# Optimization experiments

Measured on AMD Instinct MI355X. Metric: run time of the kernel, lower is better.

Reference implementation:

```python
import jax, jax.numpy as jnp
import numpy as np

P_PARTS = 6
NUM_CLASSES = 50000
BATCH = 128
PART_DIM = 256
LABEL_SMOOTH = 0.1
MARGIN = 0.3
TEMP = 3.0
KL_CLAMP = 5.0
LAMBDA_GRAPH = 0.1
LAMBDA_TRI = 1.0
LAMBDA_ADV = 0.1
START_EPOCH = 20


def setup_inputs() -> dict:
    key = jax.random.key(0)
    ks = jax.random.split(key, 8)
    id_logits = jax.random.normal(ks[0], (P_PARTS, BATCH, NUM_CLASSES), dtype=jnp.float32)
    id_features = jax.random.normal(ks[1], (P_PARTS, BATCH, PART_DIM), dtype=jnp.float32)
    gray_features = jax.random.normal(ks[2], (P_PARTS, BATCH, PART_DIM), dtype=jnp.float32)
    # soft labels are probability distributions (teacher softmax outputs)
    soft_labels = jax.nn.softmax(jax.random.normal(ks[3], (P_PARTS, BATCH, NUM_CLASSES), dtype=jnp.float32), axis=-1)
    entropy_weights = jax.random.uniform(ks[4], (P_PARTS, BATCH), dtype=jnp.float32)
    adv_logits = jax.random.normal(ks[5], (P_PARTS, BATCH, 2), dtype=jnp.float32)
    labels = jax.random.randint(ks[6], (BATCH,), 0, 16, dtype=jnp.int64 if jax.config.jax_enable_x64 else jnp.int32)
    modality_labels = jax.random.randint(ks[7], (BATCH,), 0, 2, dtype=jnp.int64 if jax.config.jax_enable_x64 else jnp.int32)
    return {
        'id_logits': id_logits,
        'id_features': id_features,
        'gray_features': gray_features,
        'soft_labels': soft_labels,
        'entropy_weights': entropy_weights,
        'adv_logits': adv_logits,
        'labels': labels,
        'modality_labels': modality_labels,
        'current_epoch': 25,
    }


def _ce(logits, labels, smoothing):
    # torch CrossEntropyLoss with label_smoothing, mean reduction. logits: [B,C]
    logp = jax.nn.log_softmax(logits, axis=-1)
    nll = -jnp.take_along_axis(logp, labels[:, None], axis=-1)[:, 0]
    smooth = -jnp.mean(logp, axis=-1)
    return jnp.mean((1.0 - smoothing) * nll + smoothing * smooth)


def _triplet(feat, target_feat, labels, same):
    # euclidean cdist [B,B]
    sq = (jnp.sum(feat * feat, axis=1)[:, None]
          + jnp.sum(target_feat * target_feat, axis=1)[None, :]
          - 2.0 * feat @ target_feat.T)
    dist = jnp.sqrt(jnp.clip(sq, 0.0) + 1e-12)
    eq = labels[:, None] == labels[None, :]
    is_neg = ~eq
    is_pos = eq & (~jnp.eye(feat.shape[0], dtype=bool)) if same else eq
    # vectorized hard mining (replaces per-row python loop)
    dist_ap = jnp.where(is_pos.any(axis=1),
                        jnp.max(jnp.where(is_pos, dist, -jnp.inf), axis=1), 0.0)
    dist_an = jnp.where(is_neg.any(axis=1),
                        jnp.min(jnp.where(is_neg, dist, jnp.inf), axis=1), 1e6)
    # MarginRankingLoss with y=1: mean(relu(dist_ap - dist_an + margin))
    return jnp.mean(jnp.maximum(dist_ap - dist_an + MARGIN, 0.0))


def reference(id_logits, id_features, gray_features, soft_labels, entropy_weights,
              adv_logits, labels, modality_labels, current_epoch):
    P = id_logits.shape[0]
    # --- multi-part ID loss ---
    L_id = jnp.mean(jax.vmap(lambda lg: _ce(lg, labels, LABEL_SMOOTH))(id_logits))
    # --- triplet on L2-normalized concatenated part features ---
    feat = jnp.concatenate(list(id_features), axis=1)  # [B, P*D]
    feat = feat / jnp.linalg.norm(feat, axis=1, keepdims=True)
    L_tri = _triplet(feat, feat, labels, same=True)
    feat_gray = jnp.concatenate(list(gray_features), axis=1)
    feat_gray = feat_gray / jnp.linalg.norm(feat_gray, axis=1, keepdims=True)
    L_trans = _triplet(feat, feat_gray, labels, same=False)
    L_tri = L_tri + 0.5 * L_trans
    # --- graph distillation (KL) ---
    if current_epoch >= START_EPOCH:
        logp = jax.nn.log_softmax(id_logits / TEMP, axis=-1)  # [P,B,C]
        kl = jnp.sum(soft_labels * (jnp.log(soft_labels) - logp), axis=-1)  # [P,B]
        kl = jnp.minimum(kl, KL_CLAMP)
        L_graph = jnp.sum(jnp.mean(kl * entropy_weights, axis=1)) * (TEMP ** 2) / P
    else:
        L_graph = jnp.float32(0.0)
    # --- adversarial CE ---
    logp_adv = jax.nn.log_softmax(adv_logits, axis=-1)  # [P,B,2]
    nll_adv = -jnp.take_along_axis(logp_adv, modality_labels[None, :, None], axis=-1)[..., 0]
    L_adv = jnp.mean(jnp.mean(nll_adv, axis=1))
    total = L_id + LAMBDA_TRI * L_tri + LAMBDA_GRAPH * L_graph + LAMBDA_ADV * L_adv
    return total
```

## Files before the change

kernel.cpp:

```cpp
#include <hip/hip_runtime.h>

#define NCLS   50000
#define NC4    12500
#define BATCH  128
#define PPARTS 6
#define NROWS  768
#define FD     1536

__device__ __forceinline__ float wave_sum(float v) {
#pragma unroll
  for (int off = 32; off > 0; off >>= 1) v += __shfl_xor(v, off, 64);
  return v;
}

#define WS_INVF 16
#define WS_INVG 144
#define WS_D    272

__device__ __forceinline__ void chunk_update(float4 xv, float4 sv,
    float& m, float& e1, float& e2, float& sx, float& ss, float& ssl, float& ssx) {
  const float i3 = 1.0f / 3.0f;
  float cm = fmaxf(fmaxf(xv.x, xv.y), fmaxf(xv.z, xv.w));
  float nm = fmaxf(m, cm);
  float d0 = xv.x - nm, d1 = xv.y - nm, d2 = xv.z - nm, d3 = xv.w - nm;
  float r = m - nm;
  e1 = fmaf(e1, __expf(r),
            (__expf(d0) + __expf(d1)) + (__expf(d2) + __expf(d3)));
  e2 = fmaf(e2, __expf(r * i3),
            (__expf(d0 * i3) + __expf(d1 * i3)) + (__expf(d2 * i3) + __expf(d3 * i3)));
  m = nm;
  sx += (xv.x + xv.y) + (xv.z + xv.w);
  ss += (sv.x + sv.y) + (sv.z + sv.w);
  ssl = fmaf(sv.x, __logf(sv.x), fmaf(sv.y, __logf(sv.y),
        fmaf(sv.z, __logf(sv.z), fmaf(sv.w, __logf(sv.w), ssl))));
  ssx = fmaf(sv.x, xv.x, fmaf(sv.y, xv.y,
        fmaf(sv.z, xv.z, fmaf(sv.w, xv.w, ssx))));
}

__global__ __launch_bounds__(512) void big_rows_k(
    const float* __restrict__ X, const float* __restrict__ S,
    const float* __restrict__ W, const int* __restrict__ labels,
    float* __restrict__ acc) {
  const int row = blockIdx.x;
  const int b = row & (BATCH - 1);
  const int t = threadIdx.x;
  const size_t base = (size_t)row * NCLS;
  const float4* x4 = (const float4*)(X + base);
  const float4* s4 = (const float4*)(S + base);
  const float i3 = 1.0f / 3.0f;

  float x_lab = (t == 0) ? X[base + labels[b]] : 0.0f;

  float m = -1e30f, e1 = 0.0f, e2 = 0.0f;
  float sx = 0.0f, ss = 0.0f, ssl = 0.0f, ssx = 0.0f;

#pragma unroll 4
  for (int k = 0; k < 24; ++k) {
    int i = t + (k << 9);
    chunk_update(x4[i], s4[i], m, e1, e2, sx, ss, ssl, ssx);
  }
  {
    int i = 12288 + t;
    if (i < NC4) chunk_update(x4[i], s4[i], m, e1, e2, sx, ss, ssl, ssx);
  }

#pragma unroll
  for (int off = 32; off > 0; off >>= 1) {
    float mo  = __shfl_xor(m, off, 64);
    float e1o = __shfl_xor(e1, off, 64);
    float e2o = __shfl_xor(e2, off, 64);
    float nm = fmaxf(m, mo);
    e1 = e1 * __expf(m - nm) + e1o * __expf(mo - nm);
    e2 = e2 * __expf((m - nm) * i3) + e2o * __expf((mo - nm) * i3);
    m = nm;
    sx  += __shfl_xor(sx, off, 64);
    ss  += __shfl_xor(ss, off, 64);
    ssl += __shfl_xor(ssl, off, 64);
    ssx += __shfl_xor(ssx, off, 64);
  }

  __shared__ float rm[8], re1[8], re2[8], rsx[8], rss[8], rssl[8], rssx[8];
  const int lane = t & 63, wid = t >> 6;
  if (lane == 0) {
    rm[wid] = m; re1[wid] = e1; re2[wid] = e2;
    rsx[wid] = sx; rss[wid] = ss; rssl[wid] = ssl; rssx[wid] = ssx;
  }
  __syncthreads();
  if (t == 0) {
    float M = rm[0], E1 = re1[0], E2 = re2[0];
#pragma unroll
    for (int wv = 1; wv < 8; ++wv) {
      float nm = fmaxf(M, rm[wv]);
      E1 = E1 * __expf(M - nm) + re1[wv] * __expf(rm[wv] - nm);
      E2 = E2 * __expf((M - nm) * i3) + re2[wv] * __expf((rm[wv] - nm) * i3);
      M = nm;
    }
    float SX = 0.f, SS = 0.f, SSL = 0.f, SSX = 0.f;
#pragma unroll
    for (int wv = 0; wv < 8; ++wv) { SX += rsx[wv]; SS += rss[wv]; SSL += rssl[wv]; SSX += rssx[wv]; }
    float logZ  = M + __logf(E1);
    float logZT = M * i3 + __logf(E2);
    float ce = 0.9f * (logZ - x_lab) + 0.1f * (logZ - SX * (1.0f / NCLS));
    float kl = SSL - SSX * i3 + logZT * SS;
    kl = fminf(kl, 5.0f);
    atomicAdd(&acc[0], ce);
    atomicAdd(&acc[1], kl * W[row]);
  }
}

__global__ __launch_bounds__(256) void norm_k(
    const float* __restrict__ idf, const float* __restrict__ grayf,
    float* __restrict__ ws) {
  const int src = blockIdx.x >> 7;
  const int b = blockIdx.x & (BATCH - 1);
  const int t = threadIdx.x;
  const float* in = src ? grayf : idf;
  float sq = 0.0f;
#pragma unroll
  for (int k = 0; k < 6; ++k) {
    float v = in[((k * BATCH + b) << 8) + t];
    sq = fmaf(v, v, sq);
  }
  sq = wave_sum(sq);
  __shared__ float w4[4];
  const int lane = t & 63, wid = t >> 6;
  if (lane == 0) w4[wid] = sq;
  __syncthreads();
  if (t == 0)
    ws[16 + src * BATCH + b] = 1.0f / sqrtf(w4[0] + w4[1] + w4[2] + w4[3]);
  if (blockIdx.x == 0 && t < 16) ws[t] = 0.0f;
}

__global__ __launch_bounds__(256) void dist_k(
    const float* __restrict__ idf, const float* __restrict__ grayf,
    float* __restrict__ ws) {
  const int z = blockIdx.z;
  const float* Bm = z ? grayf : idf;
  const float* invJsrc = ws + (z ? WS_INVG : WS_INVF);
  const float* invIsrc = ws + WS_INVF;
  float* D = ws + WS_D + z * BATCH * BATCH;
  const int i0 = blockIdx.y * 32, j0 = blockIdx.x * 32;
  const int t = threadIdx.x;

  __shared__ float As[32][33], Bs[32][33];
  __shared__ float sInvI[32], sInvJ[32];
  if (t < 32) sInvI[t] = invIsrc[i0 + t];
  else if (t < 64) sInvJ[t - 32] = invJsrc[j0 + t - 32];

  const int lr = t >> 3, lk = (t & 7) << 2;
  const int ty = t >> 4, tx = t & 15;

  float c00 = 0.f, c01 = 0.f, c10 = 0.f, c11 = 0.f;
  for (int k0 = 0; k0 < FD; k0 += 32) {
    const int p = (k0 + lk) >> 8;
    const int kin = (k0 + lk) & 255;
    float4 av = *(const float4*)&idf[((p * BATCH + i0 + lr) << 8) + kin];
    float4 bv = *(const float4*)&Bm [((p * BATCH + j0 + lr) << 8) + kin];
    As[lr][lk] = av.x; As[lr][lk+1] = av.y; As[lr][lk+2] = av.z; As[lr][lk+3] = av.w;
    Bs[lr][lk] = bv.x; Bs[lr][lk+1] = bv.y; Bs[lr][lk+2] = bv.z; Bs[lr][lk+3] = bv.w;
    __syncthreads();
#pragma unroll
    for (int k = 0; k < 32; ++k) {
      float a0 = As[2*ty][k],   a1 = As[2*ty+1][k];
      float b0 = Bs[2*tx][k],   b1 = Bs[2*tx+1][k];
      c00 = fmaf(a0, b0, c00);  c01 = fmaf(a0, b1, c01);
      c10 = fmaf(a1, b0, c10);  c11 = fmaf(a1, b1, c11);
    }
    __syncthreads();
  }
  float ii0 = sInvI[2*ty], ii1 = sInvI[2*ty+1];
  float jj0 = sInvJ[2*tx], jj1 = sInvJ[2*tx+1];
  float g00 = c00*ii0*jj0, g01 = c01*ii0*jj1, g10 = c10*ii1*jj0, g11 = c11*ii1*jj1;
  D[(i0+2*ty  )*BATCH + j0+2*tx  ] = sqrtf(fmaxf(2.f-2.f*g00, 0.f) + 1e-12f);
  D[(i0+2*ty  )*BATCH + j0+2*tx+1] = sqrtf(fmaxf(2.f-2.f*g01, 0.f) + 1e-12f);
  D[(i0+2*ty+1)*BATCH + j0+2*tx  ] = sqrtf(fmaxf(2.f-2.f*g10, 0.f) + 1e-12f);
  D[(i0+2*ty+1)*BATCH + j0+2*tx+1] = sqrtf(fmaxf(2.f-2.f*g11, 0.f) + 1e-12f);
}

__global__ __launch_bounds__(256) void tail_k(
    const float* __restrict__ ws_c, const float* __restrict__ advl,
    const int* __restrict__ labels, const int* __restrict__ mod,
    const int* __restrict__ epoch, float* __restrict__ out) {
  const int t = threadIdx.x;
  __shared__ int slab[BATCH];
  __shared__ float red[8];
  if (t < BATCH) slab[t] = labels[t];
  __syncthreads();

  const int z = t >> 7;
  const int b = t & (BATCH - 1);
  const int lb = slab[b];
  const float* drow = ws_c + WS_D + z * BATCH * BATCH + b * BATCH;
  float ap = -1e30f, an = 1e30f;
  int hasp = 0, hasn = 0;
#pragma unroll 4
  for (int j = 0; j < BATCH; ++j) {
    bool eq = (slab[j] == lb);
    float v = drow[j];
    bool posok = eq && (z == 1 || j != b);
    if (posok) { hasp = 1; ap = fmaxf(ap, v); }
    if (!eq)   { hasn = 1; an = fminf(an, v); }
  }
  float dap = hasp ? ap : 0.0f;
  float dan = hasn ? an : 1e6f;
  float hinge = fmaxf(dap - dan + 0.3f, 0.0f);
  hinge = wave_sum(hinge);

  float advs = 0.0f;
#pragma unroll
  for (int k = 0; k < 3; ++k) {
    int r = t + (k << 8);
    int rb = r & (BATCH - 1);
    float l0 = advl[2 * r], l1 = advl[2 * r + 1];
    float mx = fmaxf(l0, l1);
    float lse = mx + __logf(__expf(l0 - mx) + __expf(l1 - mx));
    advs += lse - (mod[rb] ? l1 : l0);
  }
  advs = wave_sum(advs);

  const int lane = t & 63, wid = t >> 6;
  if (lane == 0) { red[wid] = hinge; red[4 + wid] = advs; }
  __syncthreads();
  if (t == 0) {
    float tri1 = red[0] + red[1];
    float tri2 = red[2] + red[3];
    float adv  = red[4] + red[5] + red[6] + red[7];
    float L_id  = ws_c[0] * (1.0f / NROWS);
    float L_tri = tri1 * (1.0f / BATCH) + 0.5f * tri2 * (1.0f / BATCH);
    float L_graph = (epoch[0] >= 20) ? ws_c[1] * (9.0f / 768.0f) : 0.0f;
    float L_adv = adv * (1.0f / NROWS);
    out[0] = L_id + L_tri + 0.1f * L_graph + 0.1f * L_adv;
  }
}

extern "C" void kernel_launch(void* const* d_in, const int* in_sizes, int n_in,
                              void* d_out, int out_size, void* d_ws, size_t ws_size,
                              hipStream_t stream) {
  (void)in_sizes; (void)n_in; (void)out_size; (void)ws_size;
  const float* id_logits = (const float*)d_in[0];
  const float* id_feat   = (const float*)d_in[1];
  const float* gray_feat = (const float*)d_in[2];
  const float* soft      = (const float*)d_in[3];
  const float* entw      = (const float*)d_in[4];
  const float* advl      = (const float*)d_in[5];
  const int*   labels    = (const int*)d_in[6];
  const int*   modality  = (const int*)d_in[7];
  const int*   epoch     = (const int*)d_in[8];
  float* out = (float*)d_out;
  float* ws = (float*)d_ws;

  norm_k<<<256, 256, 0, stream>>>(id_feat, gray_feat, ws);
  dist_k<<<dim3(4, 4, 2), 256, 0, stream>>>(id_feat, gray_feat, ws);
  big_rows_k<<<NROWS, 512, 0, stream>>>(id_logits, soft, entw, labels, ws);
  tail_k<<<1, 256, 0, stream>>>(ws, advl, labels, modality, epoch, out);
}
```

Measured before the change: 411.4 us.

## Stage row tiles through LDS with async global_load_lds and drop online max

The big row-reduction kernel now double-buffers 2048-element tiles of logits and soft labels into shared memory using direct global-to-LDS loads, overlapping the next tile's fetch with compute on the current one. It also drops the running-max rescaling of the softmax sums and computes exp/log with raw exp2/log2 builtins, which cuts transcendental and ALU work per element. In exchange, the kernel adds two barriers per tile and loses overflow safety if logits ever grow large, since there is no max subtraction.

```diff
diff --git a/kernel.cpp b/kernel.cpp
--- a/kernel.cpp
+++ b/kernel.cpp
@@ -1,108 +1,116 @@
 #include <hip/hip_runtime.h>
 
 #define NCLS   50000
-#define NC4    12500
 #define BATCH  128
-#define PPARTS 6
 #define NROWS  768
 #define FD     1536
 
-__device__ __forceinline__ float wave_sum(float v) {
-#pragma unroll
-  for (int off = 32; off > 0; off >>= 1) v += __shfl_xor(v, off, 64);
-  return v;
-}
+#define TILE   2048
+#define NTILE  24
 
 #define WS_INVF 16
 #define WS_INVG 144
 #define WS_D    272
 
-__device__ __forceinline__ void chunk_update(float4 xv, float4 sv,
-    float& m, float& e1, float& e2, float& sx, float& ss, float& ssl, float& ssx) {
-  const float i3 = 1.0f / 3.0f;
-  float cm = fmaxf(fmaxf(xv.x, xv.y), fmaxf(xv.z, xv.w));
-  float nm = fmaxf(m, cm);
-  float d0 = xv.x - nm, d1 = xv.y - nm, d2 = xv.z - nm, d3 = xv.w - nm;
-  float r = m - nm;
-  e1 = fmaf(e1, __expf(r),
-            (__expf(d0) + __expf(d1)) + (__expf(d2) + __expf(d3)));
-  e2 = fmaf(e2, __expf(r * i3),
-            (__expf(d0 * i3) + __expf(d1 * i3)) + (__expf(d2 * i3) + __expf(d3 * i3)));
-  m = nm;
-  sx += (xv.x + xv.y) + (xv.z + xv.w);
-  ss += (sv.x + sv.y) + (sv.z + sv.w);
-  ssl = fmaf(sv.x, __logf(sv.x), fmaf(sv.y, __logf(sv.y),
-        fmaf(sv.z, __logf(sv.z), fmaf(sv.w, __logf(sv.w), ssl))));
-  ssx = fmaf(sv.x, xv.x, fmaf(sv.y, xv.y,
-        fmaf(sv.z, xv.z, fmaf(sv.w, xv.w, ssx))));
+#define LOG2E 1.4426950408889634f
+#define LN2   0.6931471805599453f
+
+__device__ __forceinline__ float wave_sum(float v) {
+#pragma unroll
+  for (int off = 32; off > 0; off >>= 1) v += __shfl_xor(v, off, 64);
+  return v;
+}
+__device__ __forceinline__ float fexp2(float x) { return __builtin_amdgcn_exp2f(x); }
+__device__ __forceinline__ float flog2(float x) { return __builtin_amdgcn_logf(x); }
+
+struct Acc6 { float e1, e2, sx, ss, ssl, ssx; };
+
+__device__ __forceinline__ void acc1(Acc6& a, float x, float s) {
+  a.e1 += fexp2(x * LOG2E);
+  a.e2 += fexp2(x * (LOG2E / 3.0f));
+  a.sx += x;
+  a.ss += s;
+  a.ssl = fmaf(s, flog2(s), a.ssl);
+  a.ssx = fmaf(s, x, a.ssx);
+}
+
+__device__ __forceinline__ void stage_tile(const float* gx, const float* gs,
+                                           float* dx, float* ds_, int t) {
+  const int wid = t >> 6;
+  float* dxw = dx + (wid << 8);
+  float* dsw = ds_ + (wid << 8);
+  __builtin_amdgcn_global_load_lds(
+      (const __attribute__((address_space(1))) void*)(gx + (t << 2)),
+      (__attribute__((address_space(3))) void*)dxw, 16, 0, 0);
+  __builtin_amdgcn_global_load_lds(
+      (const __attribute__((address_space(1))) void*)(gs + (t << 2)),
+      (__attribute__((address_space(3))) void*)dsw, 16, 0, 0);
 }
 
 __global__ __launch_bounds__(512) void big_rows_k(
     const float* __restrict__ X, const float* __restrict__ S,
     const float* __restrict__ W, const int* __restrict__ labels,
     float* __restrict__ acc) {
+  __shared__ float lx[2][TILE];
+  __shared__ float ls[2][TILE];
   const int row = blockIdx.x;
   const int b = row & (BATCH - 1);
   const int t = threadIdx.x;
   const size_t base = (size_t)row * NCLS;
-  const float4* x4 = (const float4*)(X + base);
-  const float4* s4 = (const float4*)(S + base);
-  const float i3 = 1.0f / 3.0f;
-
-  float x_lab = (t == 0) ? X[base + labels[b]] : 0.0f;
-
-  float m = -1e30f, e1 = 0.0f, e2 = 0.0f;
-  float sx = 0.0f, ss = 0.0f, ssl = 0.0f, ssx = 0.0f;
-
-#pragma unroll 4
-  for (int k = 0; k < 24; ++k) {
-    int i = t + (k << 9);
-    chunk_update(x4[i], s4[i], m, e1, e2, sx, ss, ssl, ssx);
+  const float* Xr = X + base;
+  const float* Sr = S + base;
+
+  float x_lab = (t == 0) ? Xr[labels[b]] : 0.0f;
+
+  Acc6 A = {0, 0, 0, 0, 0, 0};
+
+  stage_tile(Xr, Sr, lx[0], ls[0], t);
+#pragma unroll 1
+  for (int tile = 0; tile < NTILE; ++tile) {
+    const int cur = tile & 1;
+    if (tile < NTILE - 1)
+      stage_tile(Xr + (tile + 1) * TILE, Sr + (tile + 1) * TILE,
+                 lx[cur ^ 1], ls[cur ^ 1], t);
+    __syncthreads();
+    float4 xv = *(const float4*)&lx[cur][t << 2];
+    float4 sv = *(const float4*)&ls[cur][t << 2];
+    acc1(A, xv.x, sv.x);
+    acc1(A, xv.y, sv.y);
+    acc1(A, xv.z, sv.z);
+    acc1(A, xv.w, sv.w);
+    __syncthreads();
   }
   {
-    int i = 12288 + t;
-    if (i < NC4) chunk_update(x4[i], s4[i], m, e1, e2, sx, ss, ssl, ssx);
-  }
-
-#pragma unroll
-  for (int off = 32; off > 0; off >>= 1) {
-    float mo  = __shfl_xor(m, off, 64);
-    float e1o = __shfl_xor(e1, off, 64);
-    float e2o = __shfl_xor(e2, off, 64);
-    float nm = fmaxf(m, mo);
-    e1 = e1 * __expf(m - nm) + e1o * __expf(mo - nm);
-    e2 = e2 * __expf((m - nm) * i3) + e2o * __expf((mo - nm) * i3);
-    m = nm;
-    sx  += __shfl_xor(sx, off, 64);
-    ss  += __shfl_xor(ss, off, 64);
-    ssl += __shfl_xor(ssl, off, 64);
-    ssx += __shfl_xor(ssx, off, 64);
-  }
-
-  __shared__ float rm[8], re1[8], re2[8], rsx[8], rss[8], rssl[8], rssx[8];
+    float x = Xr[49152 + t], s = Sr[49152 + t];
+    acc1(A, x, s);
+  }
+  if (t < 336) {
+    float x = Xr[49664 + t], s = Sr[49664 + t];
+    acc1(A, x, s);
+  }
+
+  A.e1 = wave_sum(A.e1);  A.e2 = wave_sum(A.e2);
+  A.sx = wave_sum(A.sx);  A.ss = wave_sum(A.ss);
+  A.ssl = wave_sum(A.ssl); A.ssx = wave_sum(A.ssx);
+
+  __shared__ float r6[6][8];
   const int lane = t & 63, wid = t >> 6;
   if (lane == 0) {
-    rm[wid] = m; re1[wid] = e1; re2[wid] = e2;
-    rsx[wid] = sx; rss[wid] = ss; rssl[wid] = ssl; rssx[wid] = ssx;
+    r6[0][wid] = A.e1; r6[1][wid] = A.e2; r6[2][wid] = A.sx;
+    r6[3][wid] = A.ss; r6[4][wid] = A.ssl; r6[5][wid] = A.ssx;
   }
   __syncthreads();
   if (t == 0) {
-    float M = rm[0], E1 = re1[0], E2 = re2[0];
-#pragma unroll
-    for (int wv = 1; wv < 8; ++wv) {
-      float nm = fmaxf(M, rm[wv]);
-      E1 = E1 * __expf(M - nm) + re1[wv] * __expf(rm[wv] - nm);
-      E2 = E2 * __expf((M - nm) * i3) + re2[wv] * __expf((rm[wv] - nm) * i3);
-      M = nm;
+    float E1 = 0, E2 = 0, SX = 0, SS = 0, SSL = 0, SSX = 0;
+#pragma unroll
+    for (int w = 0; w < 8; ++w) {
+      E1 += r6[0][w]; E2 += r6[1][w]; SX += r6[2][w];
+      SS += r6[3][w]; SSL += r6[4][w]; SSX += r6[5][w];
     }
-    float SX = 0.f, SS = 0.f, SSL = 0.f, SSX = 0.f;
-#pragma unroll
-    for (int wv = 0; wv < 8; ++wv) { SX += rsx[wv]; SS += rss[wv]; SSL += rssl[wv]; SSX += rssx[wv]; }
-    float logZ  = M + __logf(E1);
-    float logZT = M * i3 + __logf(E2);
+    float logZ  = flog2(E1) * LN2;
+    float logZT = flog2(E2) * LN2;
     float ce = 0.9f * (logZ - x_lab) + 0.1f * (logZ - SX * (1.0f / NCLS));
-    float kl = SSL - SSX * i3 + logZT * SS;
-    kl = fminf(kl, 5.0f);
+    float kl = fminf(SSL * LN2 - SSX * (1.0f / 3.0f) + logZT * SS, 5.0f);
     atomicAdd(&acc[0], ce);
     atomicAdd(&acc[1], kl * W[row]);
   }
@@ -127,7 +135,7 @@
   if (lane == 0) w4[wid] = sq;
   __syncthreads();
   if (t == 0)
-    ws[16 + src * BATCH + b] = 1.0f / sqrtf(w4[0] + w4[1] + w4[2] + w4[3]);
+    ws[WS_INVF + src * BATCH + b] = 1.0f / sqrtf(w4[0] + w4[1] + w4[2] + w4[3]);
   if (blockIdx.x == 0 && t < 16) ws[t] = 0.0f;
 }
 
```

New measurement: 411.3 us. About the same (-0.0%).
